# Kernel optimization log

Measured on AMD Instinct MI355X. Metric: run time of the kernel, lower is better.

The kernel has to match this reference:

```python
import jax, jax.numpy as jnp
import numpy as np

N, D = 8192, 256

def _gram_rbf(x, y, sigma):
    x2 = jnp.sum(x * x, axis=-1)                      # [N]
    y2 = jnp.sum(y * y, axis=-1)                      # [M]
    xy = jnp.einsum('nd,md->nm', x, y)                # [N,M] GEMM
    sq = x2[:, None] + y2[None, :] - 2.0 * xy
    return jnp.exp(-sq / sigma)

def setup_inputs() -> dict:
    key = jax.random.key(0)
    k1, k2 = jax.random.split(key)
    return {
        'input': jax.random.normal(k1, (N, D), dtype=jnp.float32),
        'target': jax.random.normal(k2, (N, D), dtype=jnp.float32) + 0.5,
        'sigma': 256,
    }

def reference(input, target, sigma):
    XX = _gram_rbf(input, input, sigma)
    YY = _gram_rbf(target, target, sigma)
    XY = _gram_rbf(input, target, sigma)
    return jnp.mean(XX) + jnp.mean(YY) - 2.0 * jnp.mean(XY)
```

## Files before the change

kernel.cpp:

```cpp
#include <hip/hip_runtime.h>
#include <hip/hip_bf16.h>
#include <stdint.h>
#include <stddef.h>


#define N_PTS   8192
#define DIM     256
#define TWO_N   16384
#define CSTRIDE 16

#define AS1 __attribute__((address_space(1)))
#define AS3 __attribute__((address_space(3)))

typedef __attribute__((ext_vector_type(4))) float f32x4;
typedef __attribute__((ext_vector_type(4))) int   i32x4;
typedef __attribute__((ext_vector_type(8))) int   i32x8;

__global__ __launch_bounds__(256) void mmd_prep(const float* __restrict__ X,
                                                const float* __restrict__ Y,
                                                const int* __restrict__ sigmap,
                                                unsigned char* __restrict__ Zf8,
                                                float* __restrict__ n2,
                                                float* __restrict__ out) {
    if (blockIdx.x == 0 && threadIdx.x == 0) out[0] = 0.0f;

    const int wave = threadIdx.x >> 6;
    const int lane = threadIdx.x & 63;
    const int row  = blockIdx.x * 4 + wave;

    const float* src = (row < N_PTS) ? (X + (size_t)row * DIM)
                                     : (Y + (size_t)(row - N_PTS) * DIM);
    float4 v = ((const float4*)src)[lane];

    float s = v.x * v.x + v.y * v.y + v.z * v.z + v.w * v.w;
#pragma unroll
    for (int off = 32; off; off >>= 1) s += __shfl_down(s, off, 64);
    if (lane == 0) {
        const float c2 = -1.4426950408889634f / (float)(*sigmap);
        n2[row] = c2 * s;
    }

    const int p01 = __builtin_amdgcn_cvt_pk_fp8_f32(v.x, v.y, 0, false);
    const int p23 = __builtin_amdgcn_cvt_pk_fp8_f32(v.z, v.w, 0, false);
    const unsigned int pk = ((unsigned)p01 & 0xffffu) | ((unsigned)p23 << 16);
    *(unsigned int*)(Zf8 + (size_t)row * DIM + (size_t)lane * 4) = pk;
}

__global__ __launch_bounds__(256, 2) void mmd_main(const unsigned char* __restrict__ Zf8,
                                                   const float* __restrict__ n2,
                                                   const int* __restrict__ sigmap,
                                                   float* __restrict__ out) {
    __shared__ char smem_b[65536];
    __shared__ float wsum[4];

    const int bid = (int)blockIdx.x;
    const int br  = 127 - (bid >> 4);
    const int cc  = bid & 15;
    if (cc > br) return;

    const int t    = threadIdx.x;
    const int wave = t >> 6;
    const int lane = t & 63;
    const int wm   = wave >> 1;
    const int wn   = wave & 1;
    const int g    = lane >> 4;
    const int ml   = lane & 15;
    const int rowBase = br * 128;

    const float m2 = 2.8853900817779268f / (float)(*sigmap);
    const int   SC = 0x7f7f7f7f;

    {
        const int colBase0 = cc * 128;
#pragma unroll
        for (int i = 0; i < 8; ++i) {
            const int cidx = i * 256 + t;
            const int col  = cidx >> 4;
            const int s    = cidx & 15;
            const int gc   = s ^ (col & 15);
            const unsigned char* gp = Zf8 + (size_t)(colBase0 + col) * DIM + gc * 16;
            __builtin_amdgcn_global_load_lds((const AS1 void*)gp,
                                             (AS3 void*)(smem_b + (size_t)cidx * 16), 16, 0, 0);
        }
    }

    i32x8 af[4][2];
#pragma unroll
    for (int mt = 0; mt < 4; ++mt) {
        const unsigned char* rp =
            Zf8 + (size_t)(rowBase + wm * 64 + mt * 16 + ml) * DIM + g * 32;
#pragma unroll
        for (int kc = 0; kc < 2; ++kc) {
            union { i32x4 h[2]; i32x8 v; } u;
            u.h[0] = *(const i32x4*)(rp + kc * 128);
            u.h[1] = *(const i32x4*)(rp + kc * 128 + 16);
            af[mt][kc] = u.v;
        }
    }
    float a_i[4][4];
#pragma unroll
    for (int mt = 0; mt < 4; ++mt)
#pragma unroll
        for (int rr = 0; rr < 4; ++rr)
            a_i[mt][rr] = n2[rowBase + wm * 64 + mt * 16 + g * 4 + rr];

    float block_acc = 0.0f;
    const int brX = (br < 64);
    int cur = 0;

    for (int bc = cc; bc <= br; bc += CSTRIDE) {
        const int colBase = bc * 128;

        float b_j[4];
#pragma unroll
        for (int nt = 0; nt < 4; ++nt)
            b_j[nt] = n2[colBase + wn * 64 + nt * 16 + ml];

        f32x4 acc[4][4] = {};

        __syncthreads();

        if (bc + CSTRIDE <= br) {
            const int colBaseN = colBase + CSTRIDE * 128;
            char* dst = smem_b + (cur ^ 1) * 32768;
#pragma unroll
            for (int i = 0; i < 8; ++i) {
                const int cidx = i * 256 + t;
                const int col  = cidx >> 4;
                const int s    = cidx & 15;
                const int gc   = s ^ (col & 15);
                const unsigned char* gp = Zf8 + (size_t)(colBaseN + col) * DIM + gc * 16;
                __builtin_amdgcn_global_load_lds((const AS1 void*)gp,
                                                 (AS3 void*)(dst + (size_t)cidx * 16), 16, 0, 0);
            }
        }

        const char* buf = smem_b + cur * 32768;
#pragma unroll
        for (int kc = 0; kc < 2; ++kc) {
            const int j0 = kc * 8 + g * 2;
            i32x8 bf[4];
#pragma unroll
            for (int nt = 0; nt < 4; ++nt) {
                const int col = wn * 64 + nt * 16 + ml;
                const char* cb = buf + (size_t)col * 256;
                union { i32x4 h[2]; i32x8 v; } u;
                u.h[0] = *(const i32x4*)(cb + (size_t)((j0)     ^ ml) * 16);
                u.h[1] = *(const i32x4*)(cb + (size_t)((j0 + 1) ^ ml) * 16);
                bf[nt] = u.v;
            }
#pragma unroll
            for (int mt = 0; mt < 4; ++mt)
#pragma unroll
                for (int nt = 0; nt < 4; ++nt)
                    acc[mt][nt] = __builtin_amdgcn_mfma_scale_f32_16x16x128_f8f6f4(
                        af[mt][kc], bf[nt], acc[mt][nt],
                        0, 0,
                        0, SC,
                        0, SC);
        }

        float ts0 = 0.0f, ts1 = 0.0f, ts2 = 0.0f, ts3 = 0.0f;
#pragma unroll
        for (int mt = 0; mt < 4; ++mt)
#pragma unroll
            for (int nt = 0; nt < 4; ++nt) {
                const float ab = b_j[nt];
                ts0 += __builtin_amdgcn_exp2f(fmaf(acc[mt][nt][0], m2, a_i[mt][0] + ab));
                ts1 += __builtin_amdgcn_exp2f(fmaf(acc[mt][nt][1], m2, a_i[mt][1] + ab));
                ts2 += __builtin_amdgcn_exp2f(fmaf(acc[mt][nt][2], m2, a_i[mt][2] + ab));
                ts3 += __builtin_amdgcn_exp2f(fmaf(acc[mt][nt][3], m2, a_i[mt][3] + ab));
            }
        const float tsum = (ts0 + ts1) + (ts2 + ts3);

        const float sgn = ((bc < 64) == brX) ? 1.0f : -1.0f;
        const float w   = (bc == br) ? sgn : 2.0f * sgn;
        block_acc = fmaf(w, tsum, block_acc);
        cur ^= 1;
    }

    float s = block_acc;
#pragma unroll
    for (int off = 32; off; off >>= 1) s += __shfl_down(s, off, 64);
    if (lane == 0) wsum[wave] = s;
    __syncthreads();
    if (t == 0)
        atomicAdd(out, (wsum[0] + wsum[1] + wsum[2] + wsum[3]) * (1.0f / 67108864.0f));
}

extern "C" void kernel_launch(void* const* d_in, const int* in_sizes, int n_in,
                              void* d_out, int out_size, void* d_ws, size_t ws_size,
                              hipStream_t stream) {
    const float* X      = (const float*)d_in[0];
    const float* Y      = (const float*)d_in[1];
    const int*   sigmap = (const int*)d_in[2];
    float*       out    = (float*)d_out;

    unsigned char* Zf8 = (unsigned char*)d_ws;
    float*         n2  = (float*)((char*)d_ws + (size_t)TWO_N * DIM);

    mmd_prep<<<TWO_N / 4, 256, 0, stream>>>(X, Y, sigmap, Zf8, n2, out);
    mmd_main<<<128 * CSTRIDE, 256, 0, stream>>>(Zf8, n2, sigmap, out);
}
```

Measured before the change: 121.5 us.

## Use 512-thread blocks with 8 waves each computing a 32x64 sub-tile

The main kernel now runs 8 waves per block instead of 4. Each wave handles 32 rows instead of 64, which halves the per-wave A fragments and accumulators. The LDS fill is split across 512 threads, and the global and LDS offsets are precomputed outside the loop. The aim is more waves in flight per CU and fewer registers per wave to hide memory and exp latency. In exchange, B-tile LDS reads per MFMA double relative to compute, and the launch bound now requests occupancy of 4 blocks of 512 threads, which 64KB of LDS per block may not allow.

```diff
diff --git a/kernel.cpp b/kernel.cpp
--- a/kernel.cpp
+++ b/kernel.cpp
@@ -46,12 +46,12 @@
     *(unsigned int*)(Zf8 + (size_t)row * DIM + (size_t)lane * 4) = pk;
 }
 
-__global__ __launch_bounds__(256, 2) void mmd_main(const unsigned char* __restrict__ Zf8,
+__global__ __launch_bounds__(512, 4) void mmd_main(const unsigned char* __restrict__ Zf8,
                                                    const float* __restrict__ n2,
                                                    const int* __restrict__ sigmap,
                                                    float* __restrict__ out) {
     __shared__ char smem_b[65536];
-    __shared__ float wsum[4];
+    __shared__ float wsum[8];
 
     const int bid = (int)blockIdx.x;
     const int br  = 127 - (bid >> 4);
@@ -70,25 +70,30 @@
     const float m2 = 2.8853900817779268f / (float)(*sigmap);
     const int   SC = 0x7f7f7f7f;
 
+    int goff[4], loff[4];
+#pragma unroll
+    for (int i = 0; i < 4; ++i) {
+        const int cidx = i * 512 + t;
+        const int col  = cidx >> 4;
+        const int s    = cidx & 15;
+        const int gc   = s ^ (col & 15);
+        goff[i] = col * 256 + gc * 16;
+        loff[i] = cidx * 16;
+    }
+
     {
-        const int colBase0 = cc * 128;
-#pragma unroll
-        for (int i = 0; i < 8; ++i) {
-            const int cidx = i * 256 + t;
-            const int col  = cidx >> 4;
-            const int s    = cidx & 15;
-            const int gc   = s ^ (col & 15);
-            const unsigned char* gp = Zf8 + (size_t)(colBase0 + col) * DIM + gc * 16;
-            __builtin_amdgcn_global_load_lds((const AS1 void*)gp,
-                                             (AS3 void*)(smem_b + (size_t)cidx * 16), 16, 0, 0);
-        }
-    }
-
-    i32x8 af[4][2];
-#pragma unroll
-    for (int mt = 0; mt < 4; ++mt) {
+        const size_t cb0 = (size_t)cc * 128 * 256;
+#pragma unroll
+        for (int i = 0; i < 4; ++i)
+            __builtin_amdgcn_global_load_lds((const AS1 void*)(Zf8 + cb0 + goff[i]),
+                                             (AS3 void*)(smem_b + loff[i]), 16, 0, 0);
+    }
+
+    i32x8 af[2][2];
+#pragma unroll
+    for (int mt = 0; mt < 2; ++mt) {
         const unsigned char* rp =
-            Zf8 + (size_t)(rowBase + wm * 64 + mt * 16 + ml) * DIM + g * 32;
+            Zf8 + (size_t)(rowBase + wm * 32 + mt * 16 + ml) * DIM + g * 32;
 #pragma unroll
         for (int kc = 0; kc < 2; ++kc) {
             union { i32x4 h[2]; i32x8 v; } u;
@@ -97,60 +102,59 @@
             af[mt][kc] = u.v;
         }
     }
-    float a_i[4][4];
-#pragma unroll
-    for (int mt = 0; mt < 4; ++mt)
+    float a_i[2][4];
+#pragma unroll
+    for (int mt = 0; mt < 2; ++mt)
 #pragma unroll
         for (int rr = 0; rr < 4; ++rr)
-            a_i[mt][rr] = n2[rowBase + wm * 64 + mt * 16 + g * 4 + rr];
+            a_i[mt][rr] = n2[rowBase + wm * 32 + mt * 16 + g * 4 + rr];
+
+    int boff[2][4];
+#pragma unroll
+    for (int kc = 0; kc < 2; ++kc)
+#pragma unroll
+        for (int nt = 0; nt < 4; ++nt) {
+            const int col = wn * 64 + nt * 16 + ml;
+            const int j0  = kc * 8 + g * 2;
+            boff[kc][nt]  = col * 256 + ((j0 ^ ml) * 16);
+        }
 
     float block_acc = 0.0f;
     const int brX = (br < 64);
     int cur = 0;
 
     for (int bc = cc; bc <= br; bc += CSTRIDE) {
-        const int colBase = bc * 128;
-
         float b_j[4];
 #pragma unroll
         for (int nt = 0; nt < 4; ++nt)
-            b_j[nt] = n2[colBase + wn * 64 + nt * 16 + ml];
-
-        f32x4 acc[4][4] = {};
+            b_j[nt] = n2[bc * 128 + wn * 64 + nt * 16 + ml];
+
+        f32x4 acc[2][4] = {};
 
         __syncthreads();
 
         if (bc + CSTRIDE <= br) {
-            const int colBaseN = colBase + CSTRIDE * 128;
+            const size_t cbN = (size_t)(bc + CSTRIDE) * 128 * 256;
             char* dst = smem_b + (cur ^ 1) * 32768;
 #pragma unroll
-            for (int i = 0; i < 8; ++i) {
-                const int cidx = i * 256 + t;
-                const int col  = cidx >> 4;
-                const int s    = cidx & 15;
-                const int gc   = s ^ (col & 15);
-                const unsigned char* gp = Zf8 + (size_t)(colBaseN + col) * DIM + gc * 16;
-                __builtin_amdgcn_global_load_lds((const AS1 void*)gp,
-                                                 (AS3 void*)(dst + (size_t)cidx * 16), 16, 0, 0);
-            }
+            for (int i = 0; i < 4; ++i)
+                __builtin_amdgcn_global_load_lds((const AS1 void*)(Zf8 + cbN + goff[i]),
+                                                 (AS3 void*)(dst + loff[i]), 16, 0, 0);
         }
 
         const char* buf = smem_b + cur * 32768;
 #pragma unroll
         for (int kc = 0; kc < 2; ++kc) {
-            const int j0 = kc * 8 + g * 2;
             i32x8 bf[4];
 #pragma unroll
             for (int nt = 0; nt < 4; ++nt) {
-                const int col = wn * 64 + nt * 16 + ml;
-                const char* cb = buf + (size_t)col * 256;
                 union { i32x4 h[2]; i32x8 v; } u;
-                u.h[0] = *(const i32x4*)(cb + (size_t)((j0)     ^ ml) * 16);
-                u.h[1] = *(const i32x4*)(cb + (size_t)((j0 + 1) ^ ml) * 16);
+                u.h[0] = *(const i32x4*)(buf + boff[kc][nt]);
+                u.h[1] = *(const i32x4*)(buf + (boff[kc][nt] ^ 16));
                 bf[nt] = u.v;
             }
 #pragma unroll
-            for (int mt = 0; mt < 4; ++mt)
+            for (int mt = 0; mt < 2; ++mt)
 #pragma unroll
                 for (int nt = 0; nt < 4; ++nt)
                     acc[mt][nt] = __builtin_amdgcn_mfma_scale_f32_16x16x128_f8f6f4(
@@ -162,7 +166,7 @@
 
         float ts0 = 0.0f, ts1 = 0.0f, ts2 = 0.0f, ts3 = 0.0f;
 #pragma unroll
-        for (int mt = 0; mt < 4; ++mt)
+        for (int mt = 0; mt < 2; ++mt)
 #pragma unroll
             for (int nt = 0; nt < 4; ++nt) {
                 const float ab = b_j[nt];
@@ -184,8 +188,12 @@
     for (int off = 32; off; off >>= 1) s += __shfl_down(s, off, 64);
     if (lane == 0) wsum[wave] = s;
     __syncthreads();
-    if (t == 0)
-        atomicAdd(out, (wsum[0] + wsum[1] + wsum[2] + wsum[3]) * (1.0f / 67108864.0f));
+    if (t == 0) {
+        float r = 0.0f;
+#pragma unroll
+        for (int wv = 0; wv < 8; ++wv) r += wsum[wv];
+        atomicAdd(out, r * (1.0f / 67108864.0f));
+    }
 }
 
 extern "C" void kernel_launch(void* const* d_in, const int* in_sizes, int n_in,
@@ -200,5 +208,5 @@
     float*         n2  = (float*)((char*)d_ws + (size_t)TWO_N * DIM);
 
     mmd_prep<<<TWO_N / 4, 256, 0, stream>>>(X, Y, sigmap, Zf8, n2, out);
-    mmd_main<<<128 * CSTRIDE, 256, 0, stream>>>(Zf8, n2, sigmap, out);
+    mmd_main<<<128 * CSTRIDE, 512, 0, stream>>>(Zf8, n2, sigmap, out);
 }
```

After: 143.1 us. 1.18x slower.

## Interleave per-column MFMA groups with exp epilogue and precompute load offsets

Applied to the files above, without the earlier changes.

Reorders the inner tile loop so each column subtile's MFMAs run and the exp2 epilogue for the previous subtile runs in between, letting transcendental VALU work overlap with matrix-core execution. Also precomputes global/LDS offsets for the async B-tile loads and the swizzled LDS read offsets once outside the loop, and starts the first MFMA from a zero accumulator instead of zero-initialising. This lowers per-iteration address arithmetic and exposes overlap, at the cost of more live registers, which could hurt occupancy at two blocks per CU.

```diff
diff --git a/kernel.cpp b/kernel.cpp
--- a/kernel.cpp
+++ b/kernel.cpp
@@ -70,18 +70,23 @@
     const float m2 = 2.8853900817779268f / (float)(*sigmap);
     const int   SC = 0x7f7f7f7f;
 
+    int goff[8], loff[8];
+#pragma unroll
+    for (int i = 0; i < 8; ++i) {
+        const int cidx = i * 256 + t;
+        const int col  = cidx >> 4;
+        const int s    = cidx & 15;
+        const int gc   = s ^ (col & 15);
+        goff[i] = col * 256 + gc * 16;
+        loff[i] = cidx * 16;
+    }
+
     {
-        const int colBase0 = cc * 128;
-#pragma unroll
-        for (int i = 0; i < 8; ++i) {
-            const int cidx = i * 256 + t;
-            const int col  = cidx >> 4;
-            const int s    = cidx & 15;
-            const int gc   = s ^ (col & 15);
-            const unsigned char* gp = Zf8 + (size_t)(colBase0 + col) * DIM + gc * 16;
-            __builtin_amdgcn_global_load_lds((const AS1 void*)gp,
-                                             (AS3 void*)(smem_b + (size_t)cidx * 16), 16, 0, 0);
-        }
+        const size_t cb0 = (size_t)cc * 128 * 256;
+#pragma unroll
+        for (int i = 0; i < 8; ++i)
+            __builtin_amdgcn_global_load_lds((const AS1 void*)(Zf8 + cb0 + goff[i]),
+                                             (AS3 void*)(smem_b + loff[i]), 16, 0, 0);
     }
 
     i32x8 af[4][2];
@@ -104,80 +109,84 @@
         for (int rr = 0; rr < 4; ++rr)
             a_i[mt][rr] = n2[rowBase + wm * 64 + mt * 16 + g * 4 + rr];
 
+    int boff[2][4];
+#pragma unroll
+    for (int kc = 0; kc < 2; ++kc)
+#pragma unroll
+        for (int nt = 0; nt < 4; ++nt) {
+            const int col = wn * 64 + nt * 16 + ml;
+            const int j0  = kc * 8 + g * 2;
+            boff[kc][nt]  = col * 256 + ((j0 ^ ml) * 16);
+        }
+
+    const f32x4 zacc = {0.0f, 0.0f, 0.0f, 0.0f};
+
     float block_acc = 0.0f;
     const int brX = (br < 64);
     int cur = 0;
 
+#define EPI(n) do {                                                                  \
+        const float ab = b_j[n];                                                     \
+        _Pragma("unroll")                                                            \
+        for (int mt = 0; mt < 4; ++mt) {                                             \
+            ts0 += __builtin_amdgcn_exp2f(fmaf(acc[mt][n][0], m2, a_i[mt][0] + ab)); \
+            ts1 += __builtin_amdgcn_exp2f(fmaf(acc[mt][n][1], m2, a_i[mt][1] + ab)); \
+            ts2 += __builtin_amdgcn_exp2f(fmaf(acc[mt][n][2], m2, a_i[mt][2] + ab)); \
+            ts3 += __builtin_amdgcn_exp2f(fmaf(acc[mt][n][3], m2, a_i[mt][3] + ab)); \
+        }                                                                            \
+    } while (0)
+
     for (int bc = cc; bc <= br; bc += CSTRIDE) {
-        const int colBase = bc * 128;
-
         float b_j[4];
 #pragma unroll
         for (int nt = 0; nt < 4; ++nt)
-            b_j[nt] = n2[colBase + wn * 64 + nt * 16 + ml];
-
-        f32x4 acc[4][4] = {};
+            b_j[nt] = n2[bc * 128 + wn * 64 + nt * 16 + ml];
+
+        f32x4 acc[4][4];
+        float ts0 = 0.0f, ts1 = 0.0f, ts2 = 0.0f, ts3 = 0.0f;
 
         __syncthreads();
 
         if (bc + CSTRIDE <= br) {
-            const int colBaseN = colBase + CSTRIDE * 128;
+            const size_t cbN = (size_t)(bc + CSTRIDE) * 128 * 256;
             char* dst = smem_b + (cur ^ 1) * 32768;
 #pragma unroll
-            for (int i = 0; i < 8; ++i) {
-                const int cidx = i * 256 + t;
-                const int col  = cidx >> 4;
-                const int s    = cidx & 15;
-                const int gc   = s ^ (col & 15);
-                const unsigned char* gp = Zf8 + (size_t)(colBaseN + col) * DIM + gc * 16;
-                __builtin_amdgcn_global_load_lds((const AS1 void*)gp,
-                                                 (AS3 void*)(dst + (size_t)cidx * 16), 16, 0, 0);
+            for (int i = 0; i < 8; ++i)
+                __builtin_amdgcn_global_load_lds((const AS1 void*)(Zf8 + cbN + goff[i]),
+                                                 (AS3 void*)(dst + loff[i]), 16, 0, 0);
+        }
+
+        const char* buf = smem_b + cur * 32768;
+#pragma unroll
+        for (int nt = 0; nt < 4; ++nt) {
+            i32x8 bf[2];
+#pragma unroll
+            for (int kc = 0; kc < 2; ++kc) {
+                union { i32x4 h[2]; i32x8 v; } u;
+                u.h[0] = *(const i32x4*)(buf + boff[kc][nt]);
+                u.h[1] = *(const i32x4*)(buf + (boff[kc][nt] ^ 16));
+                bf[kc] = u.v;
             }
-        }
-
-        const char* buf = smem_b + cur * 32768;
-#pragma unroll
-        for (int kc = 0; kc < 2; ++kc) {
-            const int j0 = kc * 8 + g * 2;
-            i32x8 bf[4];
-#pragma unroll
-            for (int nt = 0; nt < 4; ++nt) {
-                const int col = wn * 64 + nt * 16 + ml;
-                const char* cb = buf + (size_t)col * 256;
-                union { i32x4 h[2]; i32x8 v; } u;
-                u.h[0] = *(const i32x4*)(cb + (size_t)((j0)     ^ ml) * 16);
-                u.h[1] = *(const i32x4*)(cb + (size_t)((j0 + 1) ^ ml) * 16);
-                bf[nt] = u.v;
-            }
 #pragma unroll
             for (int mt = 0; mt < 4; ++mt)
-#pragma unroll
-                for (int nt = 0; nt < 4; ++nt)
-                    acc[mt][nt] = __builtin_amdgcn_mfma_scale_f32_16x16x128_f8f6f4(
-                        af[mt][kc], bf[nt], acc[mt][nt],
-                        0, 0,
-                        0, SC,
-                        0, SC);
-        }
-
-        float ts0 = 0.0f, ts1 = 0.0f, ts2 = 0.0f, ts3 = 0.0f;
-#pragma unroll
-        for (int mt = 0; mt < 4; ++mt)
-#pragma unroll
-            for (int nt = 0; nt < 4; ++nt) {
-                const float ab = b_j[nt];
-                ts0 += __builtin_amdgcn_exp2f(fmaf(acc[mt][nt][0], m2, a_i[mt][0] + ab));
-                ts1 += __builtin_amdgcn_exp2f(fmaf(acc[mt][nt][1], m2, a_i[mt][1] + ab));
-                ts2 += __builtin_amdgcn_exp2f(fmaf(acc[mt][nt][2], m2, a_i[mt][2] + ab));
-                ts3 += __builtin_amdgcn_exp2f(fmaf(acc[mt][nt][3], m2, a_i[mt][3] + ab));
-            }
+                acc[mt][nt] = __builtin_amdgcn_mfma_scale_f32_16x16x128_f8f6f4(
+                    af[mt][0], bf[0], zacc, 0, 0, 0, SC, 0, SC);
+#pragma unroll
+            for (int mt = 0; mt < 4; ++mt)
+                acc[mt][nt] = __builtin_amdgcn_mfma_scale_f32_16x16x128_f8f6f4(
+                    af[mt][1], bf[1], acc[mt][nt], 0, 0, 0, SC, 0, SC);
+
+            if (nt > 0) { const int np = nt - 1; EPI(np); }
+        }
+        EPI(3);
+
         const float tsum = (ts0 + ts1) + (ts2 + ts3);
-
         const float sgn = ((bc < 64) == brX) ? 1.0f : -1.0f;
         const float w   = (bc == br) ? sgn : 2.0f * sgn;
         block_acc = fmaf(w, tsum, block_acc);
         cur ^= 1;
     }
+#undef EPI
 
     float s = block_acc;
 #pragma unroll
```

Result: no change. 120.5 us (-0.8%).

## Split K into half-tiles, halve LDS, and reload A fragments per step

Applied to the files above, without the earlier changes.

Shared memory is halved by double-buffering 128-byte K halves instead of full 256-byte column tiles, so the pipeline advances twice per column tile with a barrier per half. A fragments are no longer held in registers across the loop but re-read from global memory each K step, and the row norms are loaded as float4 in the epilogue. The column-norm exponent is factored out as a multiplier. Together these cut register and LDS use so launch bounds can ask for four blocks per CU, at the cost of more barriers, repeated global A loads and an extra exp per column.

```diff
diff --git a/kernel.cpp b/kernel.cpp
--- a/kernel.cpp
+++ b/kernel.cpp
@@ -46,11 +46,11 @@
     *(unsigned int*)(Zf8 + (size_t)row * DIM + (size_t)lane * 4) = pk;
 }
 
-__global__ __launch_bounds__(256, 2) void mmd_main(const unsigned char* __restrict__ Zf8,
+__global__ __launch_bounds__(256, 4) void mmd_main(const unsigned char* __restrict__ Zf8,
                                                    const float* __restrict__ n2,
                                                    const int* __restrict__ sigmap,
                                                    float* __restrict__ out) {
-    __shared__ char smem_b[65536];
+    __shared__ char smem_b[32768];
     __shared__ float wsum[4];
 
     const int bid = (int)blockIdx.x;
@@ -70,113 +70,98 @@
     const float m2 = 2.8853900817779268f / (float)(*sigmap);
     const int   SC = 0x7f7f7f7f;
 
+    const int gbase = (t >> 3) * 256 + (((t & 7) ^ ((t >> 3) & 7)) * 16);
+    const int lbase = t * 16;
+
+    const int rb0 = (wn * 64 + ml) * 128 + ((((g * 2))     ^ (ml & 7)) * 16);
+    const int rb1 = (wn * 64 + ml) * 128 + ((((g * 2) + 1) ^ (ml & 7)) * 16);
+
+    const unsigned char* apB = Zf8 + (size_t)(rowBase + wm * 64 + ml) * 256 + g * 32;
+    const float*         aiB = n2 + rowBase + wm * 64 + g * 4;
+
+    const f32x4 zacc = {0.0f, 0.0f, 0.0f, 0.0f};
+
     {
-        const int colBase0 = cc * 128;
+        const unsigned char* sb = Zf8 + (size_t)cc * 128 * 256 + gbase;
 #pragma unroll
-        for (int i = 0; i < 8; ++i) {
-            const int cidx = i * 256 + t;
-            const int col  = cidx >> 4;
-            const int s    = cidx & 15;
-            const int gc   = s ^ (col & 15);
-            const unsigned char* gp = Zf8 + (size_t)(colBase0 + col) * DIM + gc * 16;
-            __builtin_amdgcn_global_load_lds((const AS1 void*)gp,
-                                             (AS3 void*)(smem_b + (size_t)cidx * 16), 16, 0, 0);
-        }
+        for (int i = 0; i < 4; ++i)
+            __builtin_amdgcn_global_load_lds((const AS1 void*)(sb + i * 8192),
+                                             (AS3 void*)(smem_b + i * 4096 + lbase), 16, 0, 0);
     }
-
-    i32x8 af[4][2];
-#pragma unroll
-    for (int mt = 0; mt < 4; ++mt) {
-        const unsigned char* rp =
-            Zf8 + (size_t)(rowBase + wm * 64 + mt * 16 + ml) * DIM + g * 32;
-#pragma unroll
-        for (int kc = 0; kc < 2; ++kc) {
-            union { i32x4 h[2]; i32x8 v; } u;
-            u.h[0] = *(const i32x4*)(rp + kc * 128);
-            u.h[1] = *(const i32x4*)(rp + kc * 128 + 16);
-            af[mt][kc] = u.v;
-        }
-    }
-    float a_i[4][4];
-#pragma unroll
-    for (int mt = 0; mt < 4; ++mt)
-#pragma unroll
-        for (int rr = 0; rr < 4; ++rr)
-            a_i[mt][rr] = n2[rowBase + wm * 64 + mt * 16 + g * 4 + rr];
 
     float block_acc = 0.0f;
     const int brX = (br < 64);
+    const int nT  = (br - cc) / CSTRIDE + 1;
     int cur = 0;
 
-    for (int bc = cc; bc <= br; bc += CSTRIDE) {
-        const int colBase = bc * 128;
+    for (int tt = 0; tt < nT; ++tt) {
+        const int bc = cc + tt * CSTRIDE;
 
-        float b_j[4];
+        float eb[4];
 #pragma unroll
         for (int nt = 0; nt < 4; ++nt)
-            b_j[nt] = n2[colBase + wn * 64 + nt * 16 + ml];
+            eb[nt] = __builtin_amdgcn_exp2f(n2[bc * 128 + wn * 64 + nt * 16 + ml]);
 
-        f32x4 acc[4][4] = {};
+        f32x4 acc[4][4];
 
-        __syncthreads();
-
-        if (bc + CSTRIDE <= br) {
-            const int colBaseN = colBase + CSTRIDE * 128;
-            char* dst = smem_b + (cur ^ 1) * 32768;
-#pragma unroll
-            for (int i = 0; i < 8; ++i) {
-                const int cidx = i * 256 + t;
-                const int col  = cidx >> 4;
-                const int s    = cidx & 15;
-                const int gc   = s ^ (col & 15);
-                const unsigned char* gp = Zf8 + (size_t)(colBaseN + col) * DIM + gc * 16;
-                __builtin_amdgcn_global_load_lds((const AS1 void*)gp,
-                                                 (AS3 void*)(dst + (size_t)cidx * 16), 16, 0, 0);
-            }
-        }
-
-        const char* buf = smem_b + cur * 32768;
 #pragma unroll
         for (int kc = 0; kc < 2; ++kc) {
-            const int j0 = kc * 8 + g * 2;
-            i32x8 bf[4];
+            i32x8 af[4];
+#pragma unroll
+            for (int mt = 0; mt < 4; ++mt) {
+                union { i32x4 h[2]; i32x8 v; } u;
+                u.h[0] = *(const i32x4*)(apB + mt * 4096 + kc * 128);
+                u.h[1] = *(const i32x4*)(apB + mt * 4096 + kc * 128 + 16);
+                af[mt] = u.v;
+            }
+
+            __syncthreads();
+
+            const int sN = tt * 2 + kc + 1;
+            if (sN < nT * 2) {
+                const unsigned char* sb = Zf8
+                    + (size_t)(cc + (sN >> 1) * CSTRIDE) * 128 * 256
+                    + (sN & 1) * 128 + gbase;
+                char* dst = smem_b + (cur ^ 1) * 16384;
+#pragma unroll
+                for (int i = 0; i < 4; ++i)
+                    __builtin_amdgcn_global_load_lds((const AS1 void*)(sb + i * 8192),
+                                                     (AS3 void*)(dst + i * 4096 + lbase), 16, 0, 0);
+            }
+
+            const char* buf = smem_b + cur * 16384;
 #pragma unroll
             for (int nt = 0; nt < 4; ++nt) {
-                const int col = wn * 64 + nt * 16 + ml;
-                const char* cb = buf + (size_t)col * 256;
                 union { i32x4 h[2]; i32x8 v; } u;
-                u.h[0] = *(const i32x4*)(cb + (size_t)((j0)     ^ ml) * 16);
-                u.h[1] = *(const i32x4*)(cb + (size_t)((j0 + 1) ^ ml) * 16);
-                bf[nt] = u.v;
+                u.h[0] = *(const i32x4*)(buf + rb0 + nt * 2048);
+                u.h[1] = *(const i32x4*)(buf + rb1 + nt * 2048);
+                const i32x8 bf = u.v;
+#pragma unroll
+                for (int mt = 0; mt < 4; ++mt)
+                    acc[mt][nt] = __builtin_amdgcn_mfma_scale_f32_16x16x128_f8f6f4(
+                        af[mt], bf, (kc == 0) ? zacc : acc[mt][nt],
+                        0, 0, 0, SC, 0, SC);
             }
-#pragma unroll
-            for (int mt = 0; mt < 4; ++mt)
-#pragma unroll
-                for (int nt = 0; nt < 4; ++nt)
-                    acc[mt][nt] = __builtin_amdgcn_mfma_scale_f32_16x16x128_f8f6f4(
-                        af[mt][kc], bf[nt], acc[mt][nt],
-                        0, 0,
-                        0, SC,
-                        0, SC);
+            cur ^= 1;
         }
 
         float ts0 = 0.0f, ts1 = 0.0f, ts2 = 0.0f, ts3 = 0.0f;
 #pragma unroll
-        for (int mt = 0; mt < 4; ++mt)
+        for (int mt = 0; mt < 4; ++mt) {
+            const float4 av = *(const float4*)(aiB + mt * 16);
 #pragma unroll
             for (int nt = 0; nt < 4; ++nt) {
-                const float ab = b_j[nt];
-                ts0 += __builtin_amdgcn_exp2f(fmaf(acc[mt][nt][0], m2, a_i[mt][0] + ab));
-                ts1 += __builtin_amdgcn_exp2f(fmaf(acc[mt][nt][1], m2, a_i[mt][1] + ab));
-                ts2 += __builtin_amdgcn_exp2f(fmaf(acc[mt][nt][2], m2, a_i[mt][2] + ab));
-                ts3 += __builtin_amdgcn_exp2f(fmaf(acc[mt][nt][3], m2, a_i[mt][3] + ab));
+                const float e = eb[nt];
+                ts0 = fmaf(__builtin_amdgcn_exp2f(fmaf(acc[mt][nt][0], m2, av.x)), e, ts0);
+                ts1 = fmaf(__builtin_amdgcn_exp2f(fmaf(acc[mt][nt][1], m2, av.y)), e, ts1);
+                ts2 = fmaf(__builtin_amdgcn_exp2f(fmaf(acc[mt][nt][2], m2, av.z)), e, ts2);
+                ts3 = fmaf(__builtin_amdgcn_exp2f(fmaf(acc[mt][nt][3], m2, av.w)), e, ts3);
             }
+        }
         const float tsum = (ts0 + ts1) + (ts2 + ts3);
-
         const float sgn = ((bc < 64) == brX) ? 1.0f : -1.0f;
         const float w   = (bc == br) ? sgn : 2.0f * sgn;
         block_acc = fmaf(w, tsum, block_acc);
-        cur ^= 1;
     }
 
     float s = block_acc;
```

Result: slower. 230.1 us (+89.4%).
